# Optimization experiments

Hardware: AMD Instinct MI355X
Metric: run time of the kernel (lower is better)

## Reference

```python
import jax, jax.numpy as jnp
import numpy as np

N_OBJ, N_PAIR, D = 16384, 131072, 256
STEPS = 2  # cfg.MODEL.SG_HEAD.FEATURE_UPDATE_STEP


def setup_inputs() -> dict:
    key = jax.random.key(0)
    ks = jax.random.split(key, 8)
    s = 0.05
    return {
        "x_obj": jax.random.normal(ks[0], (N_OBJ, D), jnp.float32),
        "x_pred": jax.random.normal(ks[1], (N_PAIR, D), jnp.float32),
        "pair_idxs": jax.random.randint(ks[2], (N_PAIR, 2), 0, N_OBJ, dtype=jnp.int32),
        "w_e2v": jax.random.normal(ks[3], (2 * D, 1), jnp.float32) * s,
        "b_e2v": jnp.zeros((1,), jnp.float32),
        "w_v2e": jax.random.normal(ks[4], (2 * D, 1), jnp.float32) * s,
        "b_v2e": jnp.zeros((1,), jnp.float32),
        "w_ih": jax.random.normal(ks[5], (3 * D, D), jnp.float32) * s,
        "w_hh": jax.random.normal(ks[6], (3 * D, D), jnp.float32) * s,
        "b_ih": jnp.zeros((3 * D,), jnp.float32),
        "b_hh": jnp.zeros((3 * D,), jnp.float32),
    }


def _gate(unary, pair, w, b):
    # MessagePassingUnit_v1 with filter_size = gate_width = 1:
    # scalar gate = sigmoid(Linear(relu(cat([unary, pair])))) ; output = pair * gate
    g = jax.nn.sigmoid(jax.nn.relu(jnp.concatenate([unary, pair], axis=-1)) @ w + b)  # [E,1]
    return pair * g


def _gru(x, h, w_ih, w_hh, b_ih, b_hh):
    # torch.nn.GRUCell semantics
    gi = x @ w_ih.T + b_ih  # [N, 3D]
    gh = h @ w_hh.T + b_hh
    i_r, i_z, i_n = jnp.split(gi, 3, axis=-1)
    h_r, h_z, h_n = jnp.split(gh, 3, axis=-1)
    r = jax.nn.sigmoid(i_r + h_r)
    z = jax.nn.sigmoid(i_z + h_z)
    n = jnp.tanh(i_n + r * h_n)
    return (1.0 - z) * n + z * h


def reference(x_obj, x_pred, pair_idxs, w_e2v, b_e2v, w_v2e, b_v2e, w_ih, w_hh, b_ih, b_hh):
    n_obj = x_obj.shape[0]
    subj = pair_idxs[:, 0]
    obj = pair_idxs[:, 1]
    for _ in range(STEPS):
        # --- edge -> vertex messages (prepare_message with scatter maps == edge list) ---
        m_subj = _gate(x_obj[subj], x_pred, w_e2v, b_e2v)  # [E, D]
        m_obj = _gate(x_obj[obj], x_pred, w_e2v, b_e2v)
        msg_obj = (jax.ops.segment_sum(m_subj, subj, num_segments=n_obj)
                   + jax.ops.segment_sum(m_obj, obj, num_segments=n_obj))  # [N_obj, D]
        x_obj_new = _gru(msg_obj, x_obj, w_ih, w_hh, b_ih, b_hh)
        # --- vertex -> edge messages ---
        m_s2p = _gate(x_pred, x_obj[subj], w_v2e, b_v2e)  # [E, D]
        m_o2p = _gate(x_pred, x_obj[obj], w_v2e, b_v2e)
        x_pred_new = _gru(m_s2p + m_o2p, x_pred, w_ih, w_hh, b_ih, b_hh)
        x_obj, x_pred = x_obj_new, x_pred_new
    # concatenate updated object and predicate features along node axis (same D)
    return jnp.concatenate([x_obj, x_pred], axis=0)
```

## Files before the change

### kernel.cpp

```cpp
#include <hip/hip_runtime.h>
#include <hip/hip_bf16.h>

#define DIMN  256
#define NOBJ  16384
#define NPAIR 131072
#define NINC  (2 * NPAIR)

typedef float  floatx4 __attribute__((ext_vector_type(4)));
typedef __bf16 bf16x8  __attribute__((ext_vector_type(8)));
typedef unsigned int u32;

static __device__ __forceinline__ unsigned f2bf(float f) {
  unsigned u = __builtin_bit_cast(unsigned, f);
  u += 0x7FFFu + ((u >> 16) & 1u);
  return u >> 16;
}
static __device__ __forceinline__ float sigmoidf_(float x) {
  return 1.0f / (1.0f + __expf(-x));
}
static __device__ __forceinline__ float tanhf_(float x) {
  return 1.0f - 2.0f / (1.0f + __expf(2.0f * x));
}
static __device__ __forceinline__ float dot4(float4 a, float4 b) {
  return a.x*b.x + a.y*b.y + a.z*b.z + a.w*b.w;
}
static __device__ __forceinline__ float4 relu4(float4 a) {
  float4 r; r.x = fmaxf(a.x,0.f); r.y = fmaxf(a.y,0.f);
  r.z = fmaxf(a.z,0.f); r.w = fmaxf(a.w,0.f); return r;
}
static __device__ __forceinline__ floatx4 mfma16(bf16x8 a, bf16x8 b, floatx4 c) {
  return __builtin_amdgcn_mfma_f32_16x16x32_bf16(a, b, c, 0, 0, 0);
}
static __device__ __forceinline__ bf16x8 cvt8(float4 u, float4 v) {
  bf16x8 r;
  r[0] = (__bf16)u.x; r[1] = (__bf16)u.y; r[2] = (__bf16)u.z; r[3] = (__bf16)u.w;
  r[4] = (__bf16)v.x; r[5] = (__bf16)v.y; r[6] = (__bf16)v.z; r[7] = (__bf16)v.w;
  return r;
}
typedef const __attribute__((address_space(1))) u32* gas_ptr;
typedef __attribute__((address_space(3))) u32*       las_ptr;
static __device__ __forceinline__ void gload16(const void* g, void* l) {
  __builtin_amdgcn_global_load_lds((gas_ptr)g, (las_ptr)l, 16, 0, 0);
}

__global__ __launch_bounds__(256) void conv_w(const float* __restrict__ wih,
                                              const float* __restrict__ whh,
                                              unsigned short* __restrict__ out) {
  const int i    = blockIdx.x * 256 + threadIdx.x;
  const int lane = i & 63;
  const int kc   = (i >> 6) & 7;
  const int sct  = i >> 9;
  const int s    = sct % 6;
  const int ct   = sct / 6;
  const int col  = ct * 16 + (lane & 15);
  const int k0   = kc * 32 + (lane >> 4) * 8;
  const float* src = (s < 3) ? (wih + ((size_t)(s * 256 + col)) * 256 + k0)
                             : (whh + ((size_t)((s - 3) * 256 + col)) * 256 + k0);
  float4 a = ((const float4*)src)[0];
  float4 b = ((const float4*)src)[1];
  uint4 pk;
  pk.x = f2bf(a.x) | (f2bf(a.y) << 16);
  pk.y = f2bf(a.z) | (f2bf(a.w) << 16);
  pk.z = f2bf(b.x) | (f2bf(b.y) << 16);
  pk.w = f2bf(b.z) | (f2bf(b.w) << 16);
  *(uint4*)(out + (size_t)i * 8) = pk;
}

__global__ __launch_bounds__(256) void hist_kernel(const int* __restrict__ pairs,
                                                   int* __restrict__ cnt) {
  int i = blockIdx.x * 256 + threadIdx.x;
  atomicAdd(&cnt[pairs[i]], 1);
}

__global__ __launch_bounds__(1024) void scan_kernel(const int* __restrict__ cnt,
                                                    int* __restrict__ row_start,
                                                    int* __restrict__ cursor) {
  __shared__ int sums[1024];
  const int t = threadIdx.x;
  const int base = t * 16;
  int local[16];
  int s = 0;
  #pragma unroll
  for (int i = 0; i < 16; i++) { local[i] = s; s += cnt[base + i]; }
  sums[t] = s;
  __syncthreads();
  for (int off = 1; off < 1024; off <<= 1) {
    int v = (t >= off) ? sums[t - off] : 0;
    __syncthreads();
    sums[t] += v;
    __syncthreads();
  }
  const int prefix = (t == 0) ? 0 : sums[t - 1];
  #pragma unroll
  for (int i = 0; i < 16; i++) {
    int v = prefix + local[i];
    row_start[base + i] = v;
    cursor[base + i] = v;
  }
  if (t == 1023) row_start[16384] = sums[1023];
}

__global__ __launch_bounds__(256) void scatter_kernel(const int* __restrict__ pairs,
                                                      int* __restrict__ cursor,
                                                      int* __restrict__ entries) {
  int i = blockIdx.x * 256 + threadIdx.x;
  int pos = atomicAdd(&cursor[pairs[i]], 1);
  entries[pos] = i;
}

__global__ __launch_bounds__(256) void gate_kernel(
    const float* __restrict__ xobj, const float* __restrict__ xpred,
    const int* __restrict__ pairs,
    const float* __restrict__ w_e2v, const float* __restrict__ b_e2v,
    const float* __restrict__ w_v2e, const float* __restrict__ b_v2e,
    float* __restrict__ gbuf, unsigned short* __restrict__ xg)
{
  const int wave = threadIdx.x >> 6;
  const int lane = threadIdx.x & 63;
  const int p = blockIdx.x * 4 + wave;
  const int s = pairs[2*p], o = pairs[2*p+1];

  float4 vp = ((const float4*)(xpred + (size_t)p*DIMN))[lane];
  float4 vs = ((const float4*)(xobj  + (size_t)s*DIMN))[lane];
  float4 vo = ((const float4*)(xobj  + (size_t)o*DIMN))[lane];
  float4 we0 = ((const float4*)w_e2v)[lane];
  float4 we1 = ((const float4*)w_e2v)[64 + lane];
  float4 wv0 = ((const float4*)w_v2e)[lane];
  float4 wv1 = ((const float4*)w_v2e)[64 + lane];

  float4 rp = relu4(vp), rs = relu4(vs), ro = relu4(vo);
  float t0 = dot4(rs, we0);
  float t1 = dot4(ro, we0);
  float t2 = dot4(rp, we1);
  float t3 = dot4(rp, wv0);
  float t4 = dot4(rs, wv1);
  float t5 = dot4(ro, wv1);
  #pragma unroll
  for (int off = 32; off >= 1; off >>= 1) {
    t0 += __shfl_xor(t0, off); t1 += __shfl_xor(t1, off);
    t2 += __shfl_xor(t2, off); t3 += __shfl_xor(t3, off);
    t4 += __shfl_xor(t4, off); t5 += __shfl_xor(t5, off);
  }
  const float be = b_e2v[0], bv = b_v2e[0];
  const float g_s  = sigmoidf_(t0 + t2 + be);
  const float g_o  = sigmoidf_(t1 + t2 + be);
  const float g_sp = sigmoidf_(t3 + t4 + bv);
  const float g_op = sigmoidf_(t3 + t5 + bv);

  ushort4 pk;
  pk.x = (unsigned short)f2bf(vs.x*g_sp + vo.x*g_op);
  pk.y = (unsigned short)f2bf(vs.y*g_sp + vo.y*g_op);
  pk.z = (unsigned short)f2bf(vs.z*g_sp + vo.z*g_op);
  pk.w = (unsigned short)f2bf(vs.w*g_sp + vo.w*g_op);
  unsigned short* xrow = xg + (size_t)p * DIMN;
  *(ushort4*)(xrow + ((lane >> 1) ^ (p & 7)) * 8 + (lane & 1) * 4) = pk;

  if (lane == 0) { gbuf[2*p] = g_s; gbuf[2*p+1] = g_o; }
}

__global__ __launch_bounds__(256) void gather_kernel(
    const float* __restrict__ xpred, const float* __restrict__ gbuf,
    const int* __restrict__ row_start, const int* __restrict__ entries,
    unsigned short* __restrict__ msg)
{
  const int wave = threadIdx.x >> 6;
  const int lane = threadIdx.x & 63;
  const int obj = blockIdx.x * 4 + wave;
  const int s0 = row_start[obj], s1 = row_start[obj + 1];

  float4 acc = {0.f, 0.f, 0.f, 0.f};
  int inc = (s0 < s1) ? entries[s0] : 0;
  for (int e = s0; e < s1; e++) {
    int ninc = (e + 1 < s1) ? entries[e + 1] : 0;
    float g = gbuf[inc];
    float4 v = ((const float4*)(xpred + (size_t)(inc >> 1) * DIMN))[lane];
    acc.x += g * v.x; acc.y += g * v.y; acc.z += g * v.z; acc.w += g * v.w;
    inc = ninc;
  }
  ushort4 pk;
  pk.x = (unsigned short)f2bf(acc.x);
  pk.y = (unsigned short)f2bf(acc.y);
  pk.z = (unsigned short)f2bf(acc.z);
  pk.w = (unsigned short)f2bf(acc.w);
  unsigned short* mrow = msg + (size_t)obj * DIMN;
  *(ushort4*)(mrow + ((lane >> 1) ^ (obj & 7)) * 8 + (lane & 1) * 4) = pk;
}

__global__ __launch_bounds__(1024) void gru_kernel(
    const unsigned short* __restrict__ Xbf, const float* __restrict__ H,
    const unsigned short* __restrict__ Wpk,
    const float* __restrict__ b_ih, const float* __restrict__ b_hh,
    float* __restrict__ OUT)
{
  __shared__ unsigned short Xs[64 * 256];
  __shared__ unsigned short Hs[64 * 256];

  const int tid  = threadIdx.x;
  const int lane = tid & 63;
  const int wave = tid >> 6;
  const int quad = lane >> 4;
  const int l16  = lane & 15;
  const int rowBase = blockIdx.x * 64;
  const int col = wave * 16 + l16;

  const unsigned short* wb = Wpk + (size_t)wave * 24576 + lane * 8;

  {
    const unsigned short* xsrc = Xbf + (size_t)rowBase * DIMN;
    const int R0 = wave * 2;
    gload16(xsrc + (size_t)R0 * DIMN + lane * 8,        Xs + R0 * DIMN);
    gload16(xsrc + (size_t)(R0 + 32) * DIMN + lane * 8, Xs + (R0 + 32) * DIMN);
  }

  {
    const int r  = tid >> 4;
    const int c0 = tid & 15;
    const float* hr = H + (size_t)(rowBase + r) * DIMN;
    #pragma unroll
    for (int half = 0; half < 2; half++) {
      const int c  = c0 + half * 16;
      const int sw = (c ^ (r & 7)) * 8;
      float4 u = ((const float4*)hr)[2*c];
      float4 v = ((const float4*)hr)[2*c + 1];
      *(bf16x8*)(Hs + r * 256 + sw) = cvt8(u, v);
    }
  }
  __syncthreads();

  floatx4 ar[4], az[4], an[4], ah[4];
  #pragma unroll
  for (int mt = 0; mt < 4; mt++) {
    ar[mt] = (floatx4){0,0,0,0}; az[mt] = (floatx4){0,0,0,0};
    an[mt] = (floatx4){0,0,0,0}; ah[mt] = (floatx4){0,0,0,0};
  }

  #pragma unroll
  for (int kc = 0; kc < 8; kc++) {
    const unsigned short* wk = wb + kc * 512;
    bf16x8 bri = *(const bf16x8*)(wk);
    bf16x8 bzi = *(const bf16x8*)(wk +  4096);
    bf16x8 bni = *(const bf16x8*)(wk +  8192);
    bf16x8 brh = *(const bf16x8*)(wk + 12288);
    bf16x8 bzh = *(const bf16x8*)(wk + 16384);
    bf16x8 bnh = *(const bf16x8*)(wk + 20480);
    #pragma unroll
    for (int mt = 0; mt < 4; mt++) {
      const int sw = ((kc * 4 + quad) ^ (l16 & 7)) * 8;
      const int ao = (mt * 16 + l16) * 256 + sw;
      bf16x8 aX = *(const bf16x8*)(Xs + ao);
      bf16x8 aH = *(const bf16x8*)(Hs + ao);
      ar[mt] = mfma16(aX, bri, ar[mt]);
      ar[mt] = mfma16(aH, brh, ar[mt]);
      az[mt] = mfma16(aX, bzi, az[mt]);
      az[mt] = mfma16(aH, bzh, az[mt]);
      an[mt] = mfma16(aX, bni, an[mt]);
      ah[mt] = mfma16(aH, bnh, ah[mt]);
    }
  }

  const float br  = b_ih[col]       + b_hh[col];
  const float bz  = b_ih[col + 256] + b_hh[col + 256];
  const float bin = b_ih[col + 512];
  const float bhn = b_hh[col + 512];
  #pragma unroll
  for (int mt = 0; mt < 4; mt++) {
    #pragma unroll
    for (int v = 0; v < 4; v++) {
      const int m = rowBase + mt*16 + (quad << 2) + v;
      const size_t idx = (size_t)m * DIMN + col;
      const float r_ = sigmoidf_(ar[mt][v] + br);
      const float z_ = sigmoidf_(az[mt][v] + bz);
      const float n_ = tanhf_(an[mt][v] + bin + r_ * (ah[mt][v] + bhn));
      OUT[idx] = (1.0f - z_) * n_ + z_ * H[idx];
    }
  }
}

extern "C" void kernel_launch(void* const* d_in, const int* in_sizes, int n_in,
                              void* d_out, int out_size, void* d_ws, size_t ws_size,
                              hipStream_t stream) {
  const float* x_obj  = (const float*)d_in[0];
  const float* x_pred = (const float*)d_in[1];
  const int*   pairs  = (const int*)d_in[2];
  const float* w_e2v  = (const float*)d_in[3];
  const float* b_e2v  = (const float*)d_in[4];
  const float* w_v2e  = (const float*)d_in[5];
  const float* b_v2e  = (const float*)d_in[6];
  const float* w_ih   = (const float*)d_in[7];
  const float* w_hh   = (const float*)d_in[8];
  const float* b_ih   = (const float*)d_in[9];
  const float* b_hh   = (const float*)d_in[10];

  char* ws = (char*)d_ws;
  size_t off = 0;
  unsigned short* msg = (unsigned short*)(ws + off); off += (size_t)NOBJ * DIMN * 2;
  unsigned short* xg  = (unsigned short*)(ws + off); off += (size_t)NPAIR * DIMN * 2;
  unsigned short* wbf = (unsigned short*)(ws + off); off += (size_t)2 * 768 * 256 * 2;
  float* gbuf = (float*)(ws + off); off += (size_t)NINC * 4;
  int* row_start = (int*)(ws + off); off += (size_t)(NOBJ + 2) * 4;
  int* entries   = (int*)(ws + off); off += (size_t)NINC * 4;
  int* cnt    = (int*)msg;
  int* cursor = (int*)msg + NOBJ;

  float* O = (float*)d_out;
  float* P = O + (size_t)NOBJ * DIMN;

  conv_w<<<192, 256, 0, stream>>>(w_ih, w_hh, wbf);

  (void)hipMemsetAsync(cnt, 0, NOBJ * sizeof(int), stream);
  hist_kernel<<<NINC / 256, 256, 0, stream>>>(pairs, cnt);
  scan_kernel<<<1, 1024, 0, stream>>>(cnt, row_start, cursor);
  scatter_kernel<<<NINC / 256, 256, 0, stream>>>(pairs, cursor, entries);

  const float* xo_cur = x_obj;
  const float* xp_cur = x_pred;
  for (int s = 0; s < 2; s++) {
    gate_kernel<<<NPAIR / 4, 256, 0, stream>>>(xo_cur, xp_cur, pairs,
                                               w_e2v, b_e2v, w_v2e, b_v2e, gbuf, xg);
    gather_kernel<<<NOBJ / 4, 256, 0, stream>>>(xp_cur, gbuf, row_start, entries, msg);
    gru_kernel<<<NOBJ / 64, 1024, 0, stream>>>(msg, xo_cur, wbf, b_ih, b_hh, O);
    gru_kernel<<<NPAIR / 64, 1024, 0, stream>>>(xg, xp_cur, wbf, b_ih, b_hh, P);
    xo_cur = O; xp_cur = P;
  }
}
```

Before: 860.0 us.

## Merge object and predicate GRU launches, halve block size, reorder weight layout

The two GRU launches per step are merged into one grid, with predicate blocks first and object blocks after. Each 64-row tile is now split across two 512-thread blocks, each covering half of the 256 output columns, and launch bounds target 4 blocks per CU. The packed weight layout is reordered so the six gate sub-blocks for a given k-chunk sit next to each other. The MFMA loop is split into an X phase and an H phase to cut live A-fragment registers. The aim is higher occupancy, fewer launches, and better weight locality, at the cost of loading each X/H tile twice across the two column halves.

Result: slower. 881.3 us (+2.5%).

```diff
diff --git a/kernel.cpp b/kernel.cpp
--- a/kernel.cpp
+++ b/kernel.cpp
@@ -48,10 +48,11 @@
                                               unsigned short* __restrict__ out) {
   const int i    = blockIdx.x * 256 + threadIdx.x;
   const int lane = i & 63;
-  const int kc   = (i >> 6) & 7;
-  const int sct  = i >> 9;
-  const int s    = sct % 6;
-  const int ct   = sct / 6;
+  const int t    = i >> 6;
+  const int s    = t % 6;
+  const int u    = t / 6;
+  const int kc   = u & 7;
+  const int ct   = u >> 3;
   const int col  = ct * 16 + (lane & 15);
   const int k0   = kc * 32 + (lane >> 4) * 8;
   const float* src = (s < 3) ? (wih + ((size_t)(s * 256 + col)) * 256 + k0)
@@ -186,43 +187,56 @@
   *(ushort4*)(mrow + ((lane >> 1) ^ (obj & 7)) * 8 + (lane & 1) * 4) = pk;
 }
 
-__global__ __launch_bounds__(1024) void gru_kernel(
-    const unsigned short* __restrict__ Xbf, const float* __restrict__ H,
+__global__ __launch_bounds__(512, 4) void gru_kernel(
+    const unsigned short* __restrict__ Xp, const float* __restrict__ Hp,
+    float* __restrict__ OUTp,
+    const unsigned short* __restrict__ Xo, const float* __restrict__ Ho,
+    float* __restrict__ OUTo,
+    const int nPred,
     const unsigned short* __restrict__ Wpk,
-    const float* __restrict__ b_ih, const float* __restrict__ b_hh,
-    float* __restrict__ OUT)
+    const float* __restrict__ b_ih, const float* __restrict__ b_hh)
 {
-  __shared__ unsigned short Xs[64 * 256];
-  __shared__ unsigned short Hs[64 * 256];
+  __shared__ unsigned short A[2][64][256];
+
+  const int bid = blockIdx.x;
+  const unsigned short* Xbf;
+  const float* H;
+  float* OUT;
+  int tb;
+  if (bid < nPred) { Xbf = Xp; H = Hp; OUT = OUTp; tb = bid; }
+  else             { Xbf = Xo; H = Ho; OUT = OUTo; tb = bid - nPred; }
+  const int rowBase = (tb >> 1) * 64;
+  const int ch      = tb & 1;
 
   const int tid  = threadIdx.x;
   const int lane = tid & 63;
   const int wave = tid >> 6;
   const int quad = lane >> 4;
   const int l16  = lane & 15;
-  const int rowBase = blockIdx.x * 64;
-  const int col = wave * 16 + l16;
-
-  const unsigned short* wb = Wpk + (size_t)wave * 24576 + lane * 8;
+  const int ct   = ch * 8 + wave;
+  const int col  = ct * 16 + l16;
+
+  const unsigned short* wb = Wpk + (size_t)ct * 24576 + lane * 8;
 
   {
     const unsigned short* xsrc = Xbf + (size_t)rowBase * DIMN;
-    const int R0 = wave * 2;
-    gload16(xsrc + (size_t)R0 * DIMN + lane * 8,        Xs + R0 * DIMN);
-    gload16(xsrc + (size_t)(R0 + 32) * DIMN + lane * 8, Xs + (R0 + 32) * DIMN);
-  }
-
+    #pragma unroll
+    for (int i = 0; i < 4; i++) {
+      const int R = wave * 8 + i * 2;
+      gload16(xsrc + (size_t)R * DIMN + lane * 8, &A[0][R][0]);
+    }
+  }
   {
-    const int r  = tid >> 4;
-    const int c0 = tid & 15;
+    const int r  = tid >> 3;
+    const int c0 = tid & 7;
     const float* hr = H + (size_t)(rowBase + r) * DIMN;
     #pragma unroll
-    for (int half = 0; half < 2; half++) {
-      const int c  = c0 + half * 16;
+    for (int it = 0; it < 4; it++) {
+      const int c  = c0 + it * 8;
       const int sw = (c ^ (r & 7)) * 8;
       float4 u = ((const float4*)hr)[2*c];
       float4 v = ((const float4*)hr)[2*c + 1];
-      *(bf16x8*)(Hs + r * 256 + sw) = cvt8(u, v);
+      *(bf16x8*)(&A[1][r][sw]) = cvt8(u, v);
     }
   }
   __syncthreads();
@@ -236,24 +250,26 @@
 
   #pragma unroll
   for (int kc = 0; kc < 8; kc++) {
-    const unsigned short* wk = wb + kc * 512;
+    const unsigned short* wk = wb + kc * 3072;
+    const int sw = ((kc * 4 + quad) ^ (l16 & 7)) * 8;
     bf16x8 bri = *(const bf16x8*)(wk);
-    bf16x8 bzi = *(const bf16x8*)(wk +  4096);
-    bf16x8 bni = *(const bf16x8*)(wk +  8192);
-    bf16x8 brh = *(const bf16x8*)(wk + 12288);
-    bf16x8 bzh = *(const bf16x8*)(wk + 16384);
-    bf16x8 bnh = *(const bf16x8*)(wk + 20480);
+    bf16x8 bzi = *(const bf16x8*)(wk +  512);
+    bf16x8 bni = *(const bf16x8*)(wk + 1024);
     #pragma unroll
     for (int mt = 0; mt < 4; mt++) {
-      const int sw = ((kc * 4 + quad) ^ (l16 & 7)) * 8;
-      const int ao = (mt * 16 + l16) * 256 + sw;
-      bf16x8 aX = *(const bf16x8*)(Xs + ao);
-      bf16x8 aH = *(const bf16x8*)(Hs + ao);
+      bf16x8 aX = *(const bf16x8*)(&A[0][mt * 16 + l16][sw]);
       ar[mt] = mfma16(aX, bri, ar[mt]);
+      az[mt] = mfma16(aX, bzi, az[mt]);
+      an[mt] = mfma16(aX, bni, an[mt]);
+    }
+    bf16x8 brh = *(const bf16x8*)(wk + 1536);
+    bf16x8 bzh = *(const bf16x8*)(wk + 2048);
+    bf16x8 bnh = *(const bf16x8*)(wk + 2560);
+    #pragma unroll
+    for (int mt = 0; mt < 4; mt++) {
+      bf16x8 aH = *(const bf16x8*)(&A[1][mt * 16 + l16][sw]);
       ar[mt] = mfma16(aH, brh, ar[mt]);
-      az[mt] = mfma16(aX, bzi, az[mt]);
       az[mt] = mfma16(aH, bzh, az[mt]);
-      an[mt] = mfma16(aX, bni, an[mt]);
       ah[mt] = mfma16(aH, bnh, ah[mt]);
     }
   }
@@ -305,6 +321,9 @@
   float* O = (float*)d_out;
   float* P = O + (size_t)NOBJ * DIMN;
 
+  const int nPredBlk = (NPAIR / 64) * 2;
+  const int nObjBlk  = (NOBJ  / 64) * 2;
+
   conv_w<<<192, 256, 0, stream>>>(w_ih, w_hh, wbf);
 
   (void)hipMemsetAsync(cnt, 0, NOBJ * sizeof(int), stream);
@@ -318,8 +337,8 @@
     gate_kernel<<<NPAIR / 4, 256, 0, stream>>>(xo_cur, xp_cur, pairs,
                                                w_e2v, b_e2v, w_v2e, b_v2e, gbuf, xg);
     gather_kernel<<<NOBJ / 4, 256, 0, stream>>>(xp_cur, gbuf, row_start, entries, msg);
-    gru_kernel<<<NOBJ / 64, 1024, 0, stream>>>(msg, xo_cur, wbf, b_ih, b_hh, O);
-    gru_kernel<<<NPAIR / 64, 1024, 0, stream>>>(xg, xp_cur, wbf, b_ih, b_hh, P);
+    gru_kernel<<<nPredBlk + nObjBlk, 512, 0, stream>>>(
+        xg, xp_cur, P, msg, xo_cur, O, nPredBlk, wbf, b_ih, b_hh);
     xo_cur = O; xp_cur = P;
   }
 }
```

## Merge GRU launches into persistent double-buffered kernel with bf16 hidden-state staging

Applied to the files above, without the earlier changes.

Replaces the two per-step GRU launches with a single persistent kernel of 256 blocks. Each block walks a contiguous range of 32-row tiles covering both predicate and object rows, prefetching the next tile into a second LDS buffer while it computes the current one. The hidden state is pre-converted to swizzled bf16 by the gate kernel and a new conv_h kernel, so the GRU can load it asynchronously instead of converting fp32 in-kernel. The weight layout is reordered so the six gate fragments for one k-chunk sit next to each other. In exchange it adds extra bf16 buffers and global writes, and the tile count is smaller per block, which may lower MFMA reuse of the weights.

Result: slower. 1.887 ms (+119.4%).

```diff
diff --git a/kernel.cpp b/kernel.cpp
--- a/kernel.cpp
+++ b/kernel.cpp
@@ -5,6 +5,8 @@
 #define NOBJ  16384
 #define NPAIR 131072
 #define NINC  (2 * NPAIR)
+#define NPRT  (NPAIR / 32)
+#define NTILE (NPRT + NOBJ / 32)
 
 typedef float  floatx4 __attribute__((ext_vector_type(4)));
 typedef __bf16 bf16x8  __attribute__((ext_vector_type(8)));
@@ -30,12 +32,6 @@
 }
 static __device__ __forceinline__ floatx4 mfma16(bf16x8 a, bf16x8 b, floatx4 c) {
   return __builtin_amdgcn_mfma_f32_16x16x32_bf16(a, b, c, 0, 0, 0);
-}
-static __device__ __forceinline__ bf16x8 cvt8(float4 u, float4 v) {
-  bf16x8 r;
-  r[0] = (__bf16)u.x; r[1] = (__bf16)u.y; r[2] = (__bf16)u.z; r[3] = (__bf16)u.w;
-  r[4] = (__bf16)v.x; r[5] = (__bf16)v.y; r[6] = (__bf16)v.z; r[7] = (__bf16)v.w;
-  return r;
 }
 typedef const __attribute__((address_space(1))) u32* gas_ptr;
 typedef __attribute__((address_space(3))) u32*       las_ptr;
@@ -48,10 +44,11 @@
                                               unsigned short* __restrict__ out) {
   const int i    = blockIdx.x * 256 + threadIdx.x;
   const int lane = i & 63;
-  const int kc   = (i >> 6) & 7;
-  const int sct  = i >> 9;
-  const int s    = sct % 6;
-  const int ct   = sct / 6;
+  const int t    = i >> 6;
+  const int s    = t % 6;
+  const int u    = t / 6;
+  const int kc   = u & 7;
+  const int ct   = u >> 3;
   const int col  = ct * 16 + (lane & 15);
   const int k0   = kc * 32 + (lane >> 4) * 8;
   const float* src = (s < 3) ? (wih + ((size_t)(s * 256 + col)) * 256 + k0)
@@ -64,6 +61,17 @@
   pk.z = f2bf(b.x) | (f2bf(b.y) << 16);
   pk.w = f2bf(b.z) | (f2bf(b.w) << 16);
   *(uint4*)(out + (size_t)i * 8) = pk;
+}
+
+__global__ __launch_bounds__(256) void conv_h(const float* __restrict__ src,
+                                              unsigned short* __restrict__ dst) {
+  const int wave = threadIdx.x >> 6, lane = threadIdx.x & 63;
+  const int r = blockIdx.x * 4 + wave;
+  float4 v = ((const float4*)(src + (size_t)r * DIMN))[lane];
+  ushort4 pk;
+  pk.x = (unsigned short)f2bf(v.x); pk.y = (unsigned short)f2bf(v.y);
+  pk.z = (unsigned short)f2bf(v.z); pk.w = (unsigned short)f2bf(v.w);
+  *(ushort4*)(dst + (size_t)r * DIMN + ((lane >> 1) ^ (r & 7)) * 8 + (lane & 1) * 4) = pk;
 }
 
 __global__ __launch_bounds__(256) void hist_kernel(const int* __restrict__ pairs,
@@ -113,7 +121,8 @@
     const int* __restrict__ pairs,
     const float* __restrict__ w_e2v, const float* __restrict__ b_e2v,
     const float* __restrict__ w_v2e, const float* __restrict__ b_v2e,
-    float* __restrict__ gbuf, unsigned short* __restrict__ xg)
+    float* __restrict__ gbuf, unsigned short* __restrict__ xg,
+    unsigned short* __restrict__ hp)
 {
   const int wave = threadIdx.x >> 6;
   const int lane = threadIdx.x & 63;
@@ -147,13 +156,18 @@
   const float g_sp = sigmoidf_(t3 + t4 + bv);
   const float g_op = sigmoidf_(t3 + t5 + bv);
 
+  const int swo = ((lane >> 1) ^ (p & 7)) * 8 + (lane & 1) * 4;
   ushort4 pk;
   pk.x = (unsigned short)f2bf(vs.x*g_sp + vo.x*g_op);
   pk.y = (unsigned short)f2bf(vs.y*g_sp + vo.y*g_op);
   pk.z = (unsigned short)f2bf(vs.z*g_sp + vo.z*g_op);
   pk.w = (unsigned short)f2bf(vs.w*g_sp + vo.w*g_op);
-  unsigned short* xrow = xg + (size_t)p * DIMN;
-  *(ushort4*)(xrow + ((lane >> 1) ^ (p & 7)) * 8 + (lane & 1) * 4) = pk;
+  *(ushort4*)(xg + (size_t)p * DIMN + swo) = pk;
+
+  ushort4 ph;
+  ph.x = (unsigned short)f2bf(vp.x); ph.y = (unsigned short)f2bf(vp.y);
+  ph.z = (unsigned short)f2bf(vp.z); ph.w = (unsigned short)f2bf(vp.w);
+  *(ushort4*)(hp + (size_t)p * DIMN + swo) = ph;
 
   if (lane == 0) { gbuf[2*p] = g_s; gbuf[2*p+1] = g_o; }
 }
@@ -182,98 +196,105 @@
   pk.y = (unsigned short)f2bf(acc.y);
   pk.z = (unsigned short)f2bf(acc.z);
   pk.w = (unsigned short)f2bf(acc.w);
-  unsigned short* mrow = msg + (size_t)obj * DIMN;
-  *(ushort4*)(mrow + ((lane >> 1) ^ (obj & 7)) * 8 + (lane & 1) * 4) = pk;
+  *(ushort4*)(msg + (size_t)obj * DIMN +
+              ((lane >> 1) ^ (obj & 7)) * 8 + (lane & 1) * 4) = pk;
 }
 
 __global__ __launch_bounds__(1024) void gru_kernel(
-    const unsigned short* __restrict__ Xbf, const float* __restrict__ H,
+    const unsigned short* __restrict__ Xp, const unsigned short* __restrict__ Hbp,
+    const float* __restrict__ Hfp, float* __restrict__ OUTp,
+    const unsigned short* __restrict__ Xo, const unsigned short* __restrict__ Hbo,
+    const float* __restrict__ Hfo, float* __restrict__ OUTo,
     const unsigned short* __restrict__ Wpk,
-    const float* __restrict__ b_ih, const float* __restrict__ b_hh,
-    float* __restrict__ OUT)
+    const float* __restrict__ b_ih, const float* __restrict__ b_hh)
 {
-  __shared__ unsigned short Xs[64 * 256];
-  __shared__ unsigned short Hs[64 * 256];
+  __shared__ unsigned short Xs0[32 * 256], Hs0[32 * 256];
+  __shared__ unsigned short Xs1[32 * 256], Hs1[32 * 256];
 
   const int tid  = threadIdx.x;
   const int lane = tid & 63;
   const int wave = tid >> 6;
   const int quad = lane >> 4;
   const int l16  = lane & 15;
-  const int rowBase = blockIdx.x * 64;
-  const int col = wave * 16 + l16;
+  const int col  = wave * 16 + l16;
 
   const unsigned short* wb = Wpk + (size_t)wave * 24576 + lane * 8;
-
-  {
-    const unsigned short* xsrc = Xbf + (size_t)rowBase * DIMN;
-    const int R0 = wave * 2;
-    gload16(xsrc + (size_t)R0 * DIMN + lane * 8,        Xs + R0 * DIMN);
-    gload16(xsrc + (size_t)(R0 + 32) * DIMN + lane * 8, Xs + (R0 + 32) * DIMN);
-  }
-
-  {
-    const int r  = tid >> 4;
-    const int c0 = tid & 15;
-    const float* hr = H + (size_t)(rowBase + r) * DIMN;
-    #pragma unroll
-    for (int half = 0; half < 2; half++) {
-      const int c  = c0 + half * 16;
-      const int sw = (c ^ (r & 7)) * 8;
-      float4 u = ((const float4*)hr)[2*c];
-      float4 v = ((const float4*)hr)[2*c + 1];
-      *(bf16x8*)(Hs + r * 256 + sw) = cvt8(u, v);
-    }
-  }
-  __syncthreads();
-
-  floatx4 ar[4], az[4], an[4], ah[4];
-  #pragma unroll
-  for (int mt = 0; mt < 4; mt++) {
-    ar[mt] = (floatx4){0,0,0,0}; az[mt] = (floatx4){0,0,0,0};
-    an[mt] = (floatx4){0,0,0,0}; ah[mt] = (floatx4){0,0,0,0};
-  }
-
-  #pragma unroll
-  for (int kc = 0; kc < 8; kc++) {
-    const unsigned short* wk = wb + kc * 512;
-    bf16x8 bri = *(const bf16x8*)(wk);
-    bf16x8 bzi = *(const bf16x8*)(wk +  4096);
-    bf16x8 bni = *(const bf16x8*)(wk +  8192);
-    bf16x8 brh = *(const bf16x8*)(wk + 12288);
-    bf16x8 bzh = *(const bf16x8*)(wk + 16384);
-    bf16x8 bnh = *(const bf16x8*)(wk + 20480);
-    #pragma unroll
-    for (int mt = 0; mt < 4; mt++) {
-      const int sw = ((kc * 4 + quad) ^ (l16 & 7)) * 8;
-      const int ao = (mt * 16 + l16) * 256 + sw;
-      bf16x8 aX = *(const bf16x8*)(Xs + ao);
-      bf16x8 aH = *(const bf16x8*)(Hs + ao);
-      ar[mt] = mfma16(aX, bri, ar[mt]);
-      ar[mt] = mfma16(aH, brh, ar[mt]);
-      az[mt] = mfma16(aX, bzi, az[mt]);
-      az[mt] = mfma16(aH, bzh, az[mt]);
-      an[mt] = mfma16(aX, bni, an[mt]);
-      ah[mt] = mfma16(aH, bnh, ah[mt]);
-    }
-  }
 
   const float br  = b_ih[col]       + b_hh[col];
   const float bz  = b_ih[col + 256] + b_hh[col + 256];
   const float bin = b_ih[col + 512];
   const float bhn = b_hh[col + 512];
-  #pragma unroll
-  for (int mt = 0; mt < 4; mt++) {
-    #pragma unroll
-    for (int v = 0; v < 4; v++) {
-      const int m = rowBase + mt*16 + (quad << 2) + v;
-      const size_t idx = (size_t)m * DIMN + col;
-      const float r_ = sigmoidf_(ar[mt][v] + br);
-      const float z_ = sigmoidf_(az[mt][v] + bz);
-      const float n_ = tanhf_(an[mt][v] + bin + r_ * (ah[mt][v] + bhn));
-      OUT[idx] = (1.0f - z_) * n_ + z_ * H[idx];
-    }
-  }
+
+  const int t0 = blockIdx.x * (NTILE / 256);
+
+#define STAGE(T, XS, HS) do {                                            \
+    const int _t = (T);                                                  \
+    const unsigned short* _xb; const unsigned short* _hb; int _rb;       \
+    if (_t < NPRT) { _xb = Xp; _hb = Hbp; _rb = _t * 32; }               \
+    else           { _xb = Xo; _hb = Hbo; _rb = (_t - NPRT) * 32; }      \
+    const int _R = wave * 2;       \
+    gload16(_xb + (size_t)(_rb + _R) * DIMN + lane * 8, (XS) + _R * 256); \
+    gload16(_hb + (size_t)(_rb + _R) * DIMN + lane * 8, (HS) + _R * 256); \
+  } while (0)
+
+#define COMPUTE(T, XS, HS) do {                                          \
+    const int _t = (T);                                                  \
+    const float* _hf; float* _out; int _rb;                              \
+    if (_t < NPRT) { _hf = Hfp; _out = OUTp; _rb = _t * 32; }            \
+    else           { _hf = Hfo; _out = OUTo; _rb = (_t - NPRT) * 32; }   \
+    floatx4 ar0={0,0,0,0}, az0={0,0,0,0}, an0={0,0,0,0}, ah0={0,0,0,0};  \
+    floatx4 ar1={0,0,0,0}, az1={0,0,0,0}, an1={0,0,0,0}, ah1={0,0,0,0};  \
+    _Pragma("unroll")                                                    \
+    for (int kc = 0; kc < 8; kc++) {                                     \
+      const unsigned short* wk = wb + kc * 3072;                         \
+      const int sw = ((kc * 4 + quad) ^ (l16 & 7)) * 8;                  \
+      bf16x8 bri = *(const bf16x8*)(wk);                                 \
+      bf16x8 bzi = *(const bf16x8*)(wk + 512);                           \
+      bf16x8 bni = *(const bf16x8*)(wk + 1024);                          \
+      bf16x8 aX0 = *(const bf16x8*)((XS) + l16 * 256 + sw);              \
+      bf16x8 aX1 = *(const bf16x8*)((XS) + (16 + l16) * 256 + sw);       \
+      ar0 = mfma16(aX0, bri, ar0);  ar1 = mfma16(aX1, bri, ar1);         \
+      az0 = mfma16(aX0, bzi, az0);  az1 = mfma16(aX1, bzi, az1);         \
+      an0 = mfma16(aX0, bni, an0);  an1 = mfma16(aX1, bni, an1);         \
+      bf16x8 brh = *(const bf16x8*)(wk + 1536);                          \
+      bf16x8 bzh = *(const bf16x8*)(wk + 2048);                          \
+      bf16x8 bnh = *(const bf16x8*)(wk + 2560);                          \
+      bf16x8 aH0 = *(const bf16x8*)((HS) + l16 * 256 + sw);              \
+      bf16x8 aH1 = *(const bf16x8*)((HS) + (16 + l16) * 256 + sw);       \
+      ar0 = mfma16(aH0, brh, ar0);  ar1 = mfma16(aH1, brh, ar1);         \
+      az0 = mfma16(aH0, bzh, az0);  az1 = mfma16(aH1, bzh, az1);         \
+      ah0 = mfma16(aH0, bnh, ah0);  ah1 = mfma16(aH1, bnh, ah1);         \
+    }                                                                    \
+    _Pragma("unroll")                                                    \
+    for (int v = 0; v < 4; v++) {                                        \
+      { const int m = _rb + (quad << 2) + v;                             \
+        const size_t idx = (size_t)m * DIMN + col;                       \
+        const float r_ = sigmoidf_(ar0[v] + br);                         \
+        const float z_ = sigmoidf_(az0[v] + bz);                         \
+        const float n_ = tanhf_(an0[v] + bin + r_ * (ah0[v] + bhn));     \
+        _out[idx] = (1.0f - z_) * n_ + z_ * _hf[idx]; }                  \
+      { const int m = _rb + 16 + (quad << 2) + v;                        \
+        const size_t idx = (size_t)m * DIMN + col;                       \
+        const float r_ = sigmoidf_(ar1[v] + br);                         \
+        const float z_ = sigmoidf_(az1[v] + bz);                         \
+        const float n_ = tanhf_(an1[v] + bin + r_ * (ah1[v] + bhn));     \
+        _out[idx] = (1.0f - z_) * n_ + z_ * _hf[idx]; }                  \
+    }                                                                    \
+  } while (0)
+
+  STAGE(t0, Xs0, Hs0);
+  __syncthreads();
+  #pragma unroll 1
+  for (int i = 0; i < NTILE / 256; i += 2) {
+    if (i + 1 < NTILE / 256) STAGE(t0 + i + 1, Xs1, Hs1);
+    COMPUTE(t0 + i, Xs0, Hs0);
+    __syncthreads();
+    if (i + 2 < NTILE / 256) STAGE(t0 + i + 2, Xs0, Hs0);
+    COMPUTE(t0 + i + 1, Xs1, Hs1);
+    __syncthreads();
+  }
+#undef STAGE
+#undef COMPUTE
 }
 
 extern "C" void kernel_launch(void* const* d_in, const int* in_sizes, int n_in,
@@ -293,9 +314,11 @@
 
   char* ws = (char*)d_ws;
   size_t off = 0;
-  unsigned short* msg = (unsigned short*)(ws + off); off += (size_t)NOBJ * DIMN * 2;
-  unsigned short* xg  = (unsigned short*)(ws + off); off += (size_t)NPAIR * DIMN * 2;
-  unsigned short* wbf = (unsigned short*)(ws + off); off += (size_t)2 * 768 * 256 * 2;
+  unsigned short* msg   = (unsigned short*)(ws + off); off += (size_t)NOBJ * DIMN * 2;
+  unsigned short* xg    = (unsigned short*)(ws + off); off += (size_t)NPAIR * DIMN * 2;
+  unsigned short* hp_bf = (unsigned short*)(ws + off); off += (size_t)NPAIR * DIMN * 2;
+  unsigned short* ho_bf = (unsigned short*)(ws + off); off += (size_t)NOBJ * DIMN * 2;
+  unsigned short* wbf   = (unsigned short*)(ws + off); off += (size_t)2 * 768 * 256 * 2;
   float* gbuf = (float*)(ws + off); off += (size_t)NINC * 4;
   int* row_start = (int*)(ws + off); off += (size_t)(NOBJ + 2) * 4;
   int* entries   = (int*)(ws + off); off += (size_t)NINC * 4;
@@ -316,10 +339,13 @@
   const float* xp_cur = x_pred;
   for (int s = 0; s < 2; s++) {
     gate_kernel<<<NPAIR / 4, 256, 0, stream>>>(xo_cur, xp_cur, pairs,
-                                               w_e2v, b_e2v, w_v2e, b_v2e, gbuf, xg);
+                                               w_e2v, b_e2v, w_v2e, b_v2e,
+                                               gbuf, xg, hp_bf);
+    conv_h<<<NOBJ / 4, 256, 0, stream>>>(xo_cur, ho_bf);
     gather_kernel<<<NOBJ / 4, 256, 0, stream>>>(xp_cur, gbuf, row_start, entries, msg);
-    gru_kernel<<<NOBJ / 64, 1024, 0, stream>>>(msg, xo_cur, wbf, b_ih, b_hh, O);
-    gru_kernel<<<NPAIR / 64, 1024, 0, stream>>>(xg, xp_cur, wbf, b_ih, b_hh, P);
+    gru_kernel<<<256, 1024, 0, stream>>>(xg, hp_bf, xp_cur, P,
+                                         msg, ho_bf, xo_cur, O,
+                                         wbf, b_ih, b_hh);
     xo_cur = O; xp_cur = P;
   }
 }
```
